# Kernel optimization log

Hardware: AMD Instinct MI355X
Metric: run time of the kernel (lower is better)

The kernel has to match this reference:

```python
import jax, jax.numpy as jnp
import numpy as np

D = 1024
H = 16
HD = D // H  # 64
S = 2048
B = 1


def setup_inputs() -> dict:
    key = jax.random.key(0)
    ks = jax.random.split(key, 6)
    return {
        "GLO": jax.random.normal(ks[0], (B, S, D), dtype=jnp.float32),
        "LOC": jax.random.normal(ks[1], (B, S, D), dtype=jnp.float32),
        "W_q": jax.random.normal(ks[2], (H, D, HD), dtype=jnp.float32),
        "W_k": jax.random.normal(ks[3], (H, D, HD), dtype=jnp.float32),
        "W_v": jax.random.normal(ks[4], (H, D, HD), dtype=jnp.float32),
        "W_o": jax.random.normal(ks[5], (H * HD, D), dtype=jnp.float32),
    }


def _cross_attn(q_src, kv_src, W_q, W_k, W_v, W_o):
    # q_src: [B,Sq,D], kv_src: [B,Sk,D]
    b, sq, _ = q_src.shape
    Q = jnp.einsum('bsd,hde->bhse', q_src, W_q)   # [B,H,Sq,hd]
    K = jnp.einsum('bsd,hde->bhse', kv_src, W_k)  # [B,H,Sk,hd]
    V = jnp.einsum('bsd,hde->bhse', kv_src, W_v)  # [B,H,Sk,hd]
    scores = jnp.einsum('bhqe,bhke->bhqk', Q, K) / jnp.sqrt(jnp.float32(HD))
    weights = jax.nn.softmax(scores, axis=-1)
    out = jnp.einsum('bhqk,bhke->bhqe', weights, V)  # [B,H,Sq,hd]
    # Faithful to torch .view (raw memory reinterpretation, no head transpose)
    out = out.reshape(b, sq, H * HD)
    return out @ W_o  # [B,Sq,D]


def reference(GLO, LOC, W_q, W_k, W_v, W_o):
    GLO_prime = _cross_attn(GLO, LOC, W_q, W_k, W_v, W_o)
    LOC_prime = _cross_attn(LOC, GLO, W_q, W_k, W_v, W_o)
    return (GLO_prime, LOC_prime)
```

## Files before the change

### kernel.cpp

```cpp
#include <hip/hip_runtime.h>
#include <math.h>

#define S_LEN 2048
#define D_DIM 1024
#define NH 16
#define HD 64

typedef __attribute__((ext_vector_type(8))) short bf16x8;
typedef __attribute__((ext_vector_type(4))) float f32x4;

#define MFMA(a, b, c) __builtin_amdgcn_mfma_f32_16x16x32_bf16((a), (b), (c), 0, 0, 0)

__device__ __forceinline__ unsigned short f2bf(float x) {
    unsigned int u = __float_as_uint(x);
    u = (u + 0x7FFFu + ((u >> 16) & 1u)) >> 16;
    return (unsigned short)u;
}
__device__ __forceinline__ float bf2f(unsigned short b) {
    return __uint_as_float(((unsigned int)b) << 16);
}
__device__ __forceinline__ void gl_lds16(const void* g, void* l) {
    __builtin_amdgcn_global_load_lds((const __attribute__((address_space(1))) unsigned int*)g,
                                     (__attribute__((address_space(3))) unsigned int*)l, 16, 0, 0);
}

#if defined(__has_builtin)
#if __has_builtin(__builtin_amdgcn_cvt_pk_bf16_f32)
#define HAVE_CVT_PK_BF16 1
#endif
#endif
__device__ __forceinline__ unsigned pack_bf16(float a, float b) {
#ifdef HAVE_CVT_PK_BF16
    auto r = __builtin_amdgcn_cvt_pk_bf16_f32(a, b);
    unsigned u;
    __builtin_memcpy(&u, &r, 4);
    return u;
#else
    unsigned ua = __float_as_uint(a) + 0x8000u;
    unsigned ub = __float_as_uint(b) + 0x8000u;
    return __builtin_amdgcn_perm(ub, ua, 0x07060302u);
#endif
}


__global__ __launch_bounds__(256) void prep(const float* __restrict__ GLO,
                                            const float* __restrict__ LOC,
                                            const float* __restrict__ Wq,
                                            const float* __restrict__ Wk,
                                            const float* __restrict__ Wv,
                                            const float* __restrict__ Wo,
                                            unsigned short* __restrict__ Xh,
                                            unsigned short* __restrict__ Xl,
                                            unsigned short* __restrict__ Wqh,
                                            unsigned short* __restrict__ Wql,
                                            unsigned short* __restrict__ Wkh,
                                            unsigned short* __restrict__ Wkl,
                                            unsigned short* __restrict__ Wvt,
                                            unsigned short* __restrict__ Wot) {
    int idx = blockIdx.x * 256 + threadIdx.x;
    if (idx < (1 << 19)) {
        int gg = idx & 7;
        int row = (idx >> 3) & 127;
        int kblk = (idx >> 10) & 15;
        int r = (idx >> 14) * 128 + row;
        int kg = gg ^ (row & 7);
        const float* src = (r & 2048) ? LOC : GLO;
        const float* sp = src + (size_t)(r & 2047) * 1024 + kblk * 64 + kg * 8;
        float4 x0 = *(const float4*)sp;
        float4 x1 = *(const float4*)(sp + 4);
        size_t t = (size_t)idx * 8;
        ushort4 h0, l0, h1, l1;
        h0.x = f2bf(x0.x); l0.x = f2bf(x0.x - bf2f(h0.x));
        h0.y = f2bf(x0.y); l0.y = f2bf(x0.y - bf2f(h0.y));
        h0.z = f2bf(x0.z); l0.z = f2bf(x0.z - bf2f(h0.z));
        h0.w = f2bf(x0.w); l0.w = f2bf(x0.w - bf2f(h0.w));
        h1.x = f2bf(x1.x); l1.x = f2bf(x1.x - bf2f(h1.x));
        h1.y = f2bf(x1.y); l1.y = f2bf(x1.y - bf2f(h1.y));
        h1.z = f2bf(x1.z); l1.z = f2bf(x1.z - bf2f(h1.z));
        h1.w = f2bf(x1.w); l1.w = f2bf(x1.w - bf2f(h1.w));
        *(ushort4*)(Xh + t) = h0;
        *(ushort4*)(Xh + t + 4) = h1;
        *(ushort4*)(Xl + t) = l0;
        *(ushort4*)(Xl + t + 4) = l1;
    } else {
        int idx2 = idx - (1 << 19);
        int sec = idx2 >> 17;
        int j = idx2 & 0x1FFFF;
        size_t t = (size_t)j * 8;
        if (sec < 3) {
            int gg = j & 7;
            int e = (j >> 3) & 63;
            int kblk = (j >> 9) & 15;
            int head = j >> 13;
            int kg = gg ^ (e & 7);
            int d0 = kblk * 64 + kg * 8;
            const float* W = (sec == 0) ? Wq : (sec == 1) ? Wk : Wv;
            const float* wp = W + (size_t)head * 65536 + (size_t)d0 * 64 + e;
            float wv8[8];
#pragma unroll
            for (int i = 0; i < 8; ++i) wv8[i] = wp[i * 64];
            if (sec == 0) {
                ushort4 h0, l0, h1, l1;
#pragma unroll
                for (int i = 0; i < 8; ++i) {
                    float v = wv8[i] * 0.18033688011112042f;
                    unsigned short hi = f2bf(v);
                    unsigned short lo = f2bf(v - bf2f(hi));
                    if (i < 4) {
                        ((unsigned short*)&h0)[i] = hi;
                        ((unsigned short*)&l0)[i] = lo;
                    } else {
                        ((unsigned short*)&h1)[i - 4] = hi;
                        ((unsigned short*)&l1)[i - 4] = lo;
                    }
                }
                *(ushort4*)(Wqh + t) = h0;
                *(ushort4*)(Wqh + t + 4) = h1;
                *(ushort4*)(Wql + t) = l0;
                *(ushort4*)(Wql + t + 4) = l1;
            } else if (sec == 1) {
                ushort4 h0, l0, h1, l1;
#pragma unroll
                for (int i = 0; i < 8; ++i) {
                    float v = wv8[i];
                    unsigned short hi = f2bf(v);
                    unsigned short lo = f2bf(v - bf2f(hi));
                    if (i < 4) {
                        ((unsigned short*)&h0)[i] = hi;
                        ((unsigned short*)&l0)[i] = lo;
                    } else {
                        ((unsigned short*)&h1)[i - 4] = hi;
                        ((unsigned short*)&l1)[i - 4] = lo;
                    }
                }
                *(ushort4*)(Wkh + t) = h0;
                *(ushort4*)(Wkh + t + 4) = h1;
                *(ushort4*)(Wkl + t) = l0;
                *(ushort4*)(Wkl + t + 4) = l1;
            } else {
                ushort4 v0, v1;
#pragma unroll
                for (int i = 0; i < 8; ++i) {
                    unsigned short b = f2bf(wv8[i]);
                    if (i < 4)
                        ((unsigned short*)&v0)[i] = b;
                    else
                        ((unsigned short*)&v1)[i - 4] = b;
                }
                *(ushort4*)(Wvt + t) = v0;
                *(ushort4*)(Wvt + t + 4) = v1;
            }
        } else {
            int gg = j & 7;
            int col = (j >> 3) & 63;
            int kblk = (j >> 9) & 15;
            int nblk = j >> 13;
            int kg = gg ^ (col & 7);
            int k0 = kblk * 64 + kg * 8;
            int n = nblk * 64 + col;
            ushort4 v0, v1;
#pragma unroll
            for (int i = 0; i < 8; ++i) {
                unsigned short b = f2bf(Wo[(size_t)(k0 + i) * 1024 + n]);
                if (i < 4)
                    ((unsigned short*)&v0)[i] = b;
                else
                    ((unsigned short*)&v1)[i - 4] = b;
            }
            *(ushort4*)(Wot + t) = v0;
            *(ushort4*)(Wot + t + 4) = v1;
        }
    }
}

__global__ __launch_bounds__(256) void qkv_proj(const unsigned short* __restrict__ Xh,
                                                const unsigned short* __restrict__ Xl,
                                                const unsigned short* __restrict__ Wqh,
                                                const unsigned short* __restrict__ Wql,
                                                const unsigned short* __restrict__ Wkh,
                                                const unsigned short* __restrict__ Wkl,
                                                const unsigned short* __restrict__ Wvt,
                                                unsigned short* __restrict__ Qh,
                                                unsigned short* __restrict__ Ql,
                                                unsigned short* __restrict__ Kh,
                                                unsigned short* __restrict__ Kl,
                                                unsigned short* __restrict__ Vt) {
    __shared__ unsigned short lds[36864];
    const int bid = blockIdx.x;
    const int mblk = bid & 31;
    const int head = bid >> 5;
    const int tid = threadIdx.x;
    const int lane = tid & 63;
    const int w = tid >> 6;
    const int l15 = lane & 15, quad = lane >> 4;

    f32x4 aq[2][4] = {}, ak[2][4] = {}, av[2][4] = {};
    const size_t abase0 = (size_t)mblk * 131072;
    const size_t bbase0 = (size_t)head * 65536;

    for (int kb = 0; kb < 16; ++kb) {
        __syncthreads();
        {
            const size_t ab = abase0 + (size_t)kb * 8192;
            const size_t bb = bbase0 + (size_t)kb * 4096;
#pragma unroll
            for (int j = 0; j < 4; ++j) {
                int seg = j * 256 + tid;
                gl_lds16(Xh + ab + seg * 8, &lds[seg * 8]);
                gl_lds16(Xl + ab + seg * 8, &lds[8192 + seg * 8]);
            }
#pragma unroll
            for (int j = 0; j < 2; ++j) {
                int seg = j * 256 + tid;
                gl_lds16(Wqh + bb + seg * 8, &lds[16384 + seg * 8]);
                gl_lds16(Wql + bb + seg * 8, &lds[20480 + seg * 8]);
                gl_lds16(Wkh + bb + seg * 8, &lds[24576 + seg * 8]);
                gl_lds16(Wkl + bb + seg * 8, &lds[28672 + seg * 8]);
                gl_lds16(Wvt + bb + seg * 8, &lds[32768 + seg * 8]);
            }
        }
        __syncthreads();

#pragma unroll
        for (int ksub = 0; ksub < 2; ++ksub) {
            bf16x8 ah[2], al8[2];
#pragma unroll
            for (int mt = 0; mt < 2; ++mt) {
                int row = w * 32 + mt * 16 + l15;
                int g = (ksub * 4 + quad) ^ (row & 7);
                ah[mt] = *(const bf16x8*)&lds[row * 64 + g * 8];
                al8[mt] = *(const bf16x8*)&lds[8192 + row * 64 + g * 8];
            }
#pragma unroll
            for (int nt = 0; nt < 4; ++nt) {
                int col = nt * 16 + l15;
                int o = col * 64 + ((ksub * 4 + quad) ^ (col & 7)) * 8;
                bf16x8 bqh = *(const bf16x8*)&lds[16384 + o];
                bf16x8 bql = *(const bf16x8*)&lds[20480 + o];
                bf16x8 bkh = *(const bf16x8*)&lds[24576 + o];
                bf16x8 bkl = *(const bf16x8*)&lds[28672 + o];
                bf16x8 bv = *(const bf16x8*)&lds[32768 + o];
#pragma unroll
                for (int mt = 0; mt < 2; ++mt) {
                    f32x4 a = aq[mt][nt];
                    a = MFMA(ah[mt], bqh, a);
                    a = MFMA(ah[mt], bql, a);
                    a = MFMA(al8[mt], bqh, a);
                    aq[mt][nt] = a;
                    f32x4 b = ak[mt][nt];
                    b = MFMA(ah[mt], bkh, b);
                    b = MFMA(ah[mt], bkl, b);
                    b = MFMA(al8[mt], bkh, b);
                    ak[mt][nt] = b;
                    av[mt][nt] = MFMA(ah[mt], bv, av[mt][nt]);
                }
            }
        }
    }

#pragma unroll
    for (int mt = 0; mt < 2; ++mt) {
        const int rbase = mblk * 128 + w * 32 + mt * 16 + quad * 4;
#pragma unroll
        for (int nt = 0; nt < 4; ++nt) {
            const int col = head * 64 + nt * 16 + l15;
#pragma unroll
            for (int r = 0; r < 4; ++r) {
                size_t a = (size_t)(rbase + r) * D_DIM + col;
                float vq = aq[mt][nt][r];
                unsigned short hq = f2bf(vq);
                Qh[a] = hq;
                Ql[a] = f2bf(vq - bf2f(hq));
                float vk = ak[mt][nt][r];
                unsigned short hk = f2bf(vk);
                Kh[a] = hk;
                Kl[a] = f2bf(vk - bf2f(hk));
            }
            ushort4 vp;
            vp.x = f2bf(av[mt][nt][0]);
            vp.y = f2bf(av[mt][nt][1]);
            vp.z = f2bf(av[mt][nt][2]);
            vp.w = f2bf(av[mt][nt][3]);
            *(ushort4*)(Vt + (size_t)col * (2 * S_LEN) + rbase) = vp;
        }
    }
}

__global__ __launch_bounds__(256, 4) void attn_kernel(const unsigned short* __restrict__ Qh_,
                                                      const unsigned short* __restrict__ Ql_,
                                                      const unsigned short* __restrict__ Kh_,
                                                      const unsigned short* __restrict__ Kl_,
                                                      const unsigned short* __restrict__ Vt_,
                                                      unsigned short* __restrict__ Opart,
                                                      float* __restrict__ Lse) {
    __shared__ unsigned short lds[16384];
    const int bid = blockIdx.x;
    const int qblk = bid & 15;
    const int head = (bid >> 4) & 15;
    const int dir = (bid >> 8) & 1;
    const int khalf = bid >> 9;
    const int src_q = dir, src_kv = 1 - dir;

    const int tid = threadIdx.x;
    const int lane = tid & 63;
    const int w = tid >> 6;
    const int l15 = lane & 15, quad = lane >> 4;
    const int q0w = qblk * 128 + w * 32;

    const unsigned short* KhB0 =
        Kh_ + (size_t)(src_kv * S_LEN + khalf * 1024) * D_DIM + head * 64;
    const unsigned short* KlB0 =
        Kl_ + (size_t)(src_kv * S_LEN + khalf * 1024) * D_DIM + head * 64;
    const unsigned short* Vtp =
        Vt_ + (size_t)(head * 64) * (2 * S_LEN) + src_kv * S_LEN + khalf * 1024;

    auto stage = [&](int k0) {
#pragma unroll
        for (int j = 0; j < 2; ++j) {
            int i = j * 256 + tid;
            int row = i >> 3;
            int col = ((i & 7) ^ (row & 7)) * 8;
            gl_lds16(KhB0 + (size_t)(k0 + row) * D_DIM + col, &lds[i * 8]);
            gl_lds16(KlB0 + (size_t)(k0 + row) * D_DIM + col, &lds[4096 + i * 8]);
            gl_lds16(Vtp + (size_t)row * (2 * S_LEN) + k0 + col, &lds[8192 + i * 8]);
        }
    };

    bf16x8 qh[2][2], ql[2][2];
#pragma unroll
    for (int mt = 0; mt < 2; ++mt) {
        const size_t qrow =
            (size_t)(src_q * S_LEN + q0w + mt * 16 + l15) * D_DIM + head * 64 + quad * 8;
#pragma unroll
        for (int c = 0; c < 2; ++c) {
            qh[mt][c] = *(const bf16x8*)(Qh_ + qrow + c * 32);
            ql[mt][c] = *(const bf16x8*)(Ql_ + qrow + c * 32);
        }
    }

    f32x4 o[2][4] = {};
    float mi[2] = {-1e30f, -1e30f};
    float lip[2] = {0.f, 0.f};
    unsigned short* Pw = lds + 12288 + w * 1024;

    auto chunk = [&]() {
        f32x4 sa[2][4];
        __builtin_amdgcn_s_setprio(1);
#pragma unroll
        for (int kt = 0; kt < 4; ++kt) {
            const int row = kt * 16 + l15;
            const int s0 = (quad ^ (row & 7)) * 8;
            const int s1 = ((4 + quad) ^ (row & 7)) * 8;
            bf16x8 kh0 = *(const bf16x8*)&lds[row * 64 + s0];
            bf16x8 kh1 = *(const bf16x8*)&lds[row * 64 + s1];
            bf16x8 kl0 = *(const bf16x8*)&lds[4096 + row * 64 + s0];
            bf16x8 kl1 = *(const bf16x8*)&lds[4096 + row * 64 + s1];
#pragma unroll
            for (int mt = 0; mt < 2; ++mt) {
                f32x4 a = {};
                a = MFMA(kh0, qh[mt][0], a);
                a = MFMA(kh1, qh[mt][1], a);
                a = MFMA(kl0, qh[mt][0], a);
                a = MFMA(kl1, qh[mt][1], a);
                a = MFMA(kh0, ql[mt][0], a);
                a = MFMA(kh1, ql[mt][1], a);
                sa[mt][kt] = a;
            }
        }
        __builtin_amdgcn_s_setprio(0);

#pragma unroll
        for (int mt = 0; mt < 2; ++mt) {
            f32x4 t4 = __builtin_elementwise_max(__builtin_elementwise_max(sa[mt][0], sa[mt][1]),
                                                 __builtin_elementwise_max(sa[mt][2], sa[mt][3]));
            float tm = fmaxf(fmaxf(t4[0], t4[1]), fmaxf(t4[2], t4[3]));
            tm = fmaxf(tm, __shfl_xor(tm, 16, 64));
            tm = fmaxf(tm, __shfl_xor(tm, 32, 64));
            if (__ballot(tm > mi[mt])) {
                float mn = fmaxf(mi[mt], tm);
                float al = exp2f(mi[mt] - mn);
                mi[mt] = mn;
                lip[mt] *= al;
                const f32x4 alv = {al, al, al, al};
#pragma unroll
                for (int et = 0; et < 4; ++et) o[mt][et] *= alv;
            }
            const float mn = mi[mt];
            const f32x4 mnv = {mn, mn, mn, mn};
            f32x4 rs4 = {};
#pragma unroll
            for (int kt = 0; kt < 4; ++kt) {
                f32x4 p = sa[mt][kt] - mnv;
#pragma unroll
                for (int r = 0; r < 4; ++r) p[r] = exp2f(p[r]);
                rs4 += p;
                uint2 pk;
                pk.x = pack_bf16(p[0], p[1]);
                pk.y = pack_bf16(p[2], p[3]);
                int g = (kt * 2 + (quad >> 1)) ^ (l15 & 7);
                *(uint2*)&Pw[l15 * 64 + g * 8 + (quad & 1) * 4] = pk;
            }
            lip[mt] += (rs4[0] + rs4[1]) + (rs4[2] + rs4[3]);

            __builtin_amdgcn_s_setprio(1);
#pragma unroll
            for (int c = 0; c < 2; ++c) {
                bf16x8 pf = *(const bf16x8*)&Pw[l15 * 64 + (((c * 4 + quad) ^ (l15 & 7)) * 8)];
#pragma unroll
                for (int et = 0; et < 4; ++et) {
                    const int row = et * 16 + l15;
                    const int sl = ((c * 4 + quad) ^ (row & 7)) * 8;
                    bf16x8 vf = *(const bf16x8*)&lds[8192 + row * 64 + sl];
                    o[mt][et] = MFMA(vf, pf, o[mt][et]);
                }
            }
            __builtin_amdgcn_s_setprio(0);
        }
    };

#pragma unroll 1
    for (int c = 0; c < 16; ++c) {
        __syncthreads();
        stage(c * 64);
        __syncthreads();
        chunk();
    }

    const size_t pbase = (size_t)(khalf * 32 + dir * 16 + head) * 2048;
#pragma unroll
    for (int mt = 0; mt < 2; ++mt) {
        float lq = lip[mt];
        lq += __shfl_xor(lq, 16, 64);
        lq += __shfl_xor(lq, 32, 64);
        const float rl = __builtin_amdgcn_rcpf(lq);
        const int q = qblk * 128 + w * 32 + mt * 16 + l15;
        const size_t ob = (pbase + q) * 64;
#pragma unroll
        for (int et = 0; et < 4; ++et) {
            ushort4 pk;
            pk.x = f2bf(o[mt][et][0] * rl);
            pk.y = f2bf(o[mt][et][1] * rl);
            pk.z = f2bf(o[mt][et][2] * rl);
            pk.w = f2bf(o[mt][et][3] * rl);
            *(ushort4*)(Opart + ob + et * 16 + quad * 4) = pk;
        }
        if (quad == 0) Lse[pbase + q] = mi[mt] + __log2f(lq);
    }
}

__global__ __launch_bounds__(256) void combine(const unsigned short* __restrict__ Opart,
                                               const float* __restrict__ Lse,
                                               unsigned short* __restrict__ Oatt) {
    const int t = blockIdx.x * 256 + threadIdx.x;
    const int qi = t >> 3;
    const int e0 = (t & 7) * 8;
    const int dh = qi >> 11;
    const int q = qi & 2047;

    const size_t row1 = (size_t)dh * 2048 + q;
    const size_t b1 = row1 * 64 + e0;
    const size_t b2 = b1 + (size_t)4194304;
    ushort4 p1a = *(const ushort4*)(Opart + b1);
    ushort4 p1b = *(const ushort4*)(Opart + b1 + 4);
    ushort4 p2a = *(const ushort4*)(Opart + b2);
    ushort4 p2b = *(const ushort4*)(Opart + b2 + 4);
    const float l1 = Lse[row1];
    const float l2 = Lse[row1 + 65536];

    const float M = fmaxf(l1, l2);
    float w1 = exp2f(l1 - M);
    float w2 = exp2f(l2 - M);
    const float rw = __builtin_amdgcn_rcpf(w1 + w2);
    w1 *= rw;
    w2 *= rw;

    ushort4 oa, ob;
    oa.x = f2bf(bf2f(p1a.x) * w1 + bf2f(p2a.x) * w2);
    oa.y = f2bf(bf2f(p1a.y) * w1 + bf2f(p2a.y) * w2);
    oa.z = f2bf(bf2f(p1a.z) * w1 + bf2f(p2a.z) * w2);
    oa.w = f2bf(bf2f(p1a.w) * w1 + bf2f(p2a.w) * w2);
    ob.x = f2bf(bf2f(p1b.x) * w1 + bf2f(p2b.x) * w2);
    ob.y = f2bf(bf2f(p1b.y) * w1 + bf2f(p2b.y) * w2);
    ob.z = f2bf(bf2f(p1b.z) * w1 + bf2f(p2b.z) * w2);
    ob.w = f2bf(bf2f(p1b.w) * w1 + bf2f(p2b.w) * w2);

    const int rowit = q >> 4;
    const int g = ((e0 >> 3) ^ (rowit & 7)) & 7;
    const size_t oaddr =
        (size_t)dh * 131072 + (size_t)(q & 15) * 8192 + (size_t)rowit * 64 + g * 8;
    *(ushort4*)(Oatt + oaddr) = oa;
    *(ushort4*)(Oatt + oaddr + 4) = ob;
}

__global__ __launch_bounds__(256) void oproj(const unsigned short* __restrict__ Oatt,
                                             const unsigned short* __restrict__ Wot,
                                             float* __restrict__ out) {
    __shared__ unsigned short lds[24576];
    const int bid = blockIdx.x;
    const int nblk = bid & 15;
    const int mblk = bid >> 4;
    const int tid = threadIdx.x;
    const int lane = tid & 63, w = tid >> 6, l15 = lane & 15, quad = lane >> 4;

    f32x4 acc[2][4] = {};
    const size_t abase = (size_t)mblk * 131072;
    const size_t bbase = (size_t)nblk * 65536;

    auto ostage = [&](int kb, int boff) {
#pragma unroll
        for (int j = 0; j < 4; ++j) {
            int seg = j * 256 + tid;
            gl_lds16(Oatt + abase + (size_t)kb * 8192 + seg * 8, &lds[boff + seg * 8]);
        }
#pragma unroll
        for (int j = 0; j < 2; ++j) {
            int seg = j * 256 + tid;
            gl_lds16(Wot + bbase + (size_t)kb * 4096 + seg * 8, &lds[boff + 8192 + seg * 8]);
        }
    };

    auto compute = [&](int boff) {
#pragma unroll
        for (int ksub = 0; ksub < 2; ++ksub) {
            bf16x8 a[2];
#pragma unroll
            for (int mt = 0; mt < 2; ++mt) {
                int row = w * 32 + mt * 16 + l15;
                a[mt] =
                    *(const bf16x8*)&lds[boff + row * 64 + (((ksub * 4 + quad) ^ (row & 7)) * 8)];
            }
#pragma unroll
            for (int nt = 0; nt < 4; ++nt) {
                int col = nt * 16 + l15;
                bf16x8 b = *(const bf16x8*)&lds[boff + 8192 + col * 64 +
                                                (((ksub * 4 + quad) ^ (col & 7)) * 8)];
#pragma unroll
                for (int mt = 0; mt < 2; ++mt) acc[mt][nt] = MFMA(a[mt], b, acc[mt][nt]);
            }
        }
    };

    ostage(0, 0);
#pragma unroll 1
    for (int kb = 0; kb < 16; kb += 2) {
        __syncthreads();
        if (kb + 1 < 16) ostage(kb + 1, 12288);
        compute(0);
        __syncthreads();
        if (kb + 2 < 16) ostage(kb + 2, 0);
        compute(12288);
    }

#pragma unroll
    for (int mt = 0; mt < 2; ++mt) {
        const int rbase = mblk * 128 + w * 32 + mt * 16 + quad * 4;
#pragma unroll
        for (int nt = 0; nt < 4; ++nt)
#pragma unroll
            for (int r = 0; r < 4; ++r)
                out[(size_t)(rbase + r) * D_DIM + nblk * 64 + nt * 16 + l15] = acc[mt][nt][r];
    }
}

extern "C" void kernel_launch(void* const* d_in, const int* in_sizes, int n_in, void* d_out,
                              int out_size, void* d_ws, size_t ws_size, hipStream_t stream) {
    const float* GLO = (const float*)d_in[0];
    const float* LOC = (const float*)d_in[1];
    const float* Wq = (const float*)d_in[2];
    const float* Wk = (const float*)d_in[3];
    const float* Wv = (const float*)d_in[4];
    const float* Wo = (const float*)d_in[5];
    float* out = (float*)d_out;

    unsigned short* ws = (unsigned short*)d_ws;
    unsigned short* Xh = ws + 0;
    unsigned short* Xl = ws + 4194304;
    unsigned short* Wqh = ws + 8388608;
    unsigned short* Wql = ws + 9437184;
    unsigned short* Wkh = ws + 10485760;
    unsigned short* Wkl = ws + 11534336;
    unsigned short* Wvt = ws + 12582912;
    unsigned short* Wot = ws + 13631488;
    unsigned short* Qh = ws + 14680064;
    unsigned short* Ql = ws + 18874368;
    unsigned short* Kh = ws + 23068672;
    unsigned short* Kl = ws + 27262976;
    unsigned short* Vt = ws + 31457280;
    unsigned short* Oatt = ws + 35651584;
    unsigned short* Opart = ws + 0;
    float* LseP = (float*)(ws + 8388608);

    prep<<<4096, 256, 0, stream>>>(GLO, LOC, Wq, Wk, Wv, Wo, Xh, Xl, Wqh, Wql, Wkh, Wkl, Wvt, Wot);
    qkv_proj<<<512, 256, 0, stream>>>(Xh, Xl, Wqh, Wql, Wkh, Wkl, Wvt, Qh, Ql, Kh, Kl, Vt);
    attn_kernel<<<1024, 256, 0, stream>>>(Qh, Ql, Kh, Kl, Vt, Opart, LseP);
    combine<<<2048, 256, 0, stream>>>(Opart, LseP, Oatt);
    oproj<<<512, 256, 0, stream>>>(Oatt, Wot, out);
}
```

Baseline: 269.7 us.

## Double-buffer K/V tiles in attention with 32-key chunks and one barrier per step

Restructures the attention main loop to prefetch the next K chunk (32 keys) and V chunk (64 keys) into alternate LDS buffers, so there is one barrier per iteration instead of two and global loads overlap compute. The chunk size for scores drops to 32 keys, which halves P scratch and puts V fragments in registers. The block index mapping also changes so consecutive blocks share the same q block and differ in head, direction and key half, which changes L2 reuse. LDS per block grows, and the online-softmax rescale check now runs twice as often.

```diff
diff --git a/kernel.cpp b/kernel.cpp
--- a/kernel.cpp
+++ b/kernel.cpp
@@ -293,12 +293,13 @@
                                                       const unsigned short* __restrict__ Vt_,
                                                       unsigned short* __restrict__ Opart,
                                                       float* __restrict__ Lse) {
-    __shared__ unsigned short lds[16384];
+    __shared__ unsigned short lds[18432];
     const int bid = blockIdx.x;
-    const int qblk = bid & 15;
-    const int head = (bid >> 4) & 15;
-    const int dir = (bid >> 8) & 1;
-    const int khalf = bid >> 9;
+    const int rlow = bid & 63;
+    const int head = rlow & 15;
+    const int dir = (rlow >> 4) & 1;
+    const int khalf = rlow >> 5;
+    const int qblk = bid >> 6;
     const int src_q = dir, src_kv = 1 - dir;
 
     const int tid = threadIdx.x;
@@ -314,15 +315,19 @@
     const unsigned short* Vtp =
         Vt_ + (size_t)(head * 64) * (2 * S_LEN) + src_kv * S_LEN + khalf * 1024;
 
-    auto stage = [&](int k0) {
+    const int rowK = tid >> 3;
+    const int colK = ((tid & 7) ^ (rowK & 7)) * 8;
+    auto stageK = [&](int k0, int kboff) {
+        gl_lds16(KhB0 + (size_t)(k0 + rowK) * D_DIM + colK, &lds[kboff + tid * 8]);
+        gl_lds16(KlB0 + (size_t)(k0 + rowK) * D_DIM + colK, &lds[kboff + 2048 + tid * 8]);
+    };
+    auto stageV = [&](int v0, int vboff) {
 #pragma unroll
         for (int j = 0; j < 2; ++j) {
             int i = j * 256 + tid;
             int row = i >> 3;
             int col = ((i & 7) ^ (row & 7)) * 8;
-            gl_lds16(KhB0 + (size_t)(k0 + row) * D_DIM + col, &lds[i * 8]);
-            gl_lds16(KlB0 + (size_t)(k0 + row) * D_DIM + col, &lds[4096 + i * 8]);
-            gl_lds16(Vtp + (size_t)row * (2 * S_LEN) + k0 + col, &lds[8192 + i * 8]);
+            gl_lds16(Vtp + (size_t)row * (2 * S_LEN) + v0 + col, &lds[vboff + i * 8]);
         }
     };
 
@@ -341,20 +346,30 @@
     f32x4 o[2][4] = {};
     float mi[2] = {-1e30f, -1e30f};
     float lip[2] = {0.f, 0.f};
-    unsigned short* Pw = lds + 12288 + w * 1024;
-
-    auto chunk = [&]() {
-        f32x4 sa[2][4];
+    unsigned short* Pw = lds + 16384 + w * 512;
+
+    stageK(0, 0);
+    stageV(0, 8192);
+#pragma unroll 1
+    for (int kd = 0; kd < 32; ++kd) {
+        __syncthreads();
+        if (kd + 1 < 32) stageK((kd + 1) * 32, (kd & 1) ? 0 : 4096);
+        if (!(kd & 1) && (kd / 2 + 1 < 16)) stageV((kd / 2 + 1) * 64, (kd & 2) ? 8192 : 12288);
+        const int kb = (kd & 1) ? 4096 : 0;
+        const int vb = ((kd >> 1) & 1) ? 12288 : 8192;
+        const int p = kd & 1;
+
+        f32x4 sa[2][2];
         __builtin_amdgcn_s_setprio(1);
 #pragma unroll
-        for (int kt = 0; kt < 4; ++kt) {
+        for (int kt = 0; kt < 2; ++kt) {
             const int row = kt * 16 + l15;
             const int s0 = (quad ^ (row & 7)) * 8;
             const int s1 = ((4 + quad) ^ (row & 7)) * 8;
-            bf16x8 kh0 = *(const bf16x8*)&lds[row * 64 + s0];
-            bf16x8 kh1 = *(const bf16x8*)&lds[row * 64 + s1];
-            bf16x8 kl0 = *(const bf16x8*)&lds[4096 + row * 64 + s0];
-            bf16x8 kl1 = *(const bf16x8*)&lds[4096 + row * 64 + s1];
+            bf16x8 kh0 = *(const bf16x8*)&lds[kb + row * 64 + s0];
+            bf16x8 kh1 = *(const bf16x8*)&lds[kb + row * 64 + s1];
+            bf16x8 kl0 = *(const bf16x8*)&lds[kb + 2048 + row * 64 + s0];
+            bf16x8 kl1 = *(const bf16x8*)&lds[kb + 2048 + row * 64 + s1];
 #pragma unroll
             for (int mt = 0; mt < 2; ++mt) {
                 f32x4 a = {};
@@ -369,10 +384,16 @@
         }
         __builtin_amdgcn_s_setprio(0);
 
+        bf16x8 vf[4];
+#pragma unroll
+        for (int et = 0; et < 4; ++et) {
+            const int row = et * 16 + l15;
+            vf[et] = *(const bf16x8*)&lds[vb + row * 64 + (((p * 4 + quad) ^ (row & 7)) * 8)];
+        }
+
 #pragma unroll
         for (int mt = 0; mt < 2; ++mt) {
-            f32x4 t4 = __builtin_elementwise_max(__builtin_elementwise_max(sa[mt][0], sa[mt][1]),
-                                                 __builtin_elementwise_max(sa[mt][2], sa[mt][3]));
+            f32x4 t4 = __builtin_elementwise_max(sa[mt][0], sa[mt][1]);
             float tm = fmaxf(fmaxf(t4[0], t4[1]), fmaxf(t4[2], t4[3]));
             tm = fmaxf(tm, __shfl_xor(tm, 16, 64));
             tm = fmaxf(tm, __shfl_xor(tm, 32, 64));
@@ -389,41 +410,25 @@
             const f32x4 mnv = {mn, mn, mn, mn};
             f32x4 rs4 = {};
 #pragma unroll
-            for (int kt = 0; kt < 4; ++kt) {
-                f32x4 p = sa[mt][kt] - mnv;
-#pragma unroll
-                for (int r = 0; r < 4; ++r) p[r] = exp2f(p[r]);
-                rs4 += p;
+            for (int kt = 0; kt < 2; ++kt) {
+                f32x4 pv = sa[mt][kt] - mnv;
+#pragma unroll
+                for (int r = 0; r < 4; ++r) pv[r] = exp2f(pv[r]);
+                rs4 += pv;
                 uint2 pk;
-                pk.x = pack_bf16(p[0], p[1]);
-                pk.y = pack_bf16(p[2], p[3]);
-                int g = (kt * 2 + (quad >> 1)) ^ (l15 & 7);
-                *(uint2*)&Pw[l15 * 64 + g * 8 + (quad & 1) * 4] = pk;
+                pk.x = pack_bf16(pv[0], pv[1]);
+                pk.y = pack_bf16(pv[2], pv[3]);
+                int g = (kt * 2 + (quad >> 1)) ^ (l15 & 3);
+                *(uint2*)&Pw[l15 * 32 + g * 8 + (quad & 1) * 4] = pk;
             }
             lip[mt] += (rs4[0] + rs4[1]) + (rs4[2] + rs4[3]);
 
+            bf16x8 pf = *(const bf16x8*)&Pw[l15 * 32 + ((quad ^ (l15 & 3)) * 8)];
             __builtin_amdgcn_s_setprio(1);
 #pragma unroll
-            for (int c = 0; c < 2; ++c) {
-                bf16x8 pf = *(const bf16x8*)&Pw[l15 * 64 + (((c * 4 + quad) ^ (l15 & 7)) * 8)];
-#pragma unroll
-                for (int et = 0; et < 4; ++et) {
-                    const int row = et * 16 + l15;
-                    const int sl = ((c * 4 + quad) ^ (row & 7)) * 8;
-                    bf16x8 vf = *(const bf16x8*)&lds[8192 + row * 64 + sl];
-                    o[mt][et] = MFMA(vf, pf, o[mt][et]);
-                }
-            }
+            for (int et = 0; et < 4; ++et) o[mt][et] = MFMA(vf[et], pf, o[mt][et]);
             __builtin_amdgcn_s_setprio(0);
         }
-    };
-
-#pragma unroll 1
-    for (int c = 0; c < 16; ++c) {
-        __syncthreads();
-        stage(c * 64);
-        __syncthreads();
-        chunk();
     }
 
     const size_t pbase = (size_t)(khalf * 32 + dir * 16 + head) * 2048;
```

Result: faster. 263.2 us (-2.4%).

## Double-buffer attention K/V staging with 512-thread blocks and lazy softmax rescale

Applied to the files above, without the earlier changes.

The attention kernel moves to 512-thread blocks covering 256 queries, with a double-buffered LDS ring, so the next K/V chunk's global-to-LDS load overlaps the current chunk's compute. Each block's K/V chunk is now shared by twice as many query rows. Online-softmax rescaling is skipped unless the running max grows by more than 8 (log2 units), which cuts rescale work but lets exponentials reach up to 2^8 before rescaling. The block-index mapping is reordered in both the attention and o-projection kernels, presumably to improve cache locality, and the setprio hints are removed. The doubled LDS and larger blocks may lower occupancy.

```diff
diff --git a/kernel.cpp b/kernel.cpp
--- a/kernel.cpp
+++ b/kernel.cpp
@@ -286,26 +286,26 @@
     }
 }
 
-__global__ __launch_bounds__(256, 4) void attn_kernel(const unsigned short* __restrict__ Qh_,
+__global__ __launch_bounds__(512, 4) void attn_kernel(const unsigned short* __restrict__ Qh_,
                                                       const unsigned short* __restrict__ Ql_,
                                                       const unsigned short* __restrict__ Kh_,
                                                       const unsigned short* __restrict__ Kl_,
                                                       const unsigned short* __restrict__ Vt_,
                                                       unsigned short* __restrict__ Opart,
                                                       float* __restrict__ Lse) {
-    __shared__ unsigned short lds[16384];
+    __shared__ unsigned short lds[32768];
     const int bid = blockIdx.x;
-    const int qblk = bid & 15;
-    const int head = (bid >> 4) & 15;
-    const int dir = (bid >> 8) & 1;
-    const int khalf = bid >> 9;
+    const int head = bid & 15;
+    const int dir = (bid >> 4) & 1;
+    const int khalf = (bid >> 5) & 1;
+    const int qblk = bid >> 6;
     const int src_q = dir, src_kv = 1 - dir;
 
     const int tid = threadIdx.x;
     const int lane = tid & 63;
     const int w = tid >> 6;
     const int l15 = lane & 15, quad = lane >> 4;
-    const int q0w = qblk * 128 + w * 32;
+    const int q0w = qblk * 256 + w * 32;
 
     const unsigned short* KhB0 =
         Kh_ + (size_t)(src_kv * S_LEN + khalf * 1024) * D_DIM + head * 64;
@@ -314,16 +314,16 @@
     const unsigned short* Vtp =
         Vt_ + (size_t)(head * 64) * (2 * S_LEN) + src_kv * S_LEN + khalf * 1024;
 
-    auto stage = [&](int k0) {
-#pragma unroll
-        for (int j = 0; j < 2; ++j) {
-            int i = j * 256 + tid;
-            int row = i >> 3;
-            int col = ((i & 7) ^ (row & 7)) * 8;
-            gl_lds16(KhB0 + (size_t)(k0 + row) * D_DIM + col, &lds[i * 8]);
-            gl_lds16(KlB0 + (size_t)(k0 + row) * D_DIM + col, &lds[4096 + i * 8]);
-            gl_lds16(Vtp + (size_t)row * (2 * S_LEN) + k0 + col, &lds[8192 + i * 8]);
-        }
+    const int i0 = tid;
+    const int sr0 = i0 >> 3, sc0 = ((i0 & 7) ^ (sr0 & 7)) * 8;
+
+    auto stage = [&](int k0, int boff) {
+        const unsigned short* KhB = KhB0 + (size_t)k0 * D_DIM;
+        const unsigned short* KlB = KlB0 + (size_t)k0 * D_DIM;
+        const unsigned short* VB = Vtp + k0;
+        gl_lds16(KhB + (size_t)sr0 * D_DIM + sc0, &lds[boff + i0 * 8]);
+        gl_lds16(KlB + (size_t)sr0 * D_DIM + sc0, &lds[boff + 4096 + i0 * 8]);
+        gl_lds16(VB + (size_t)sr0 * (2 * S_LEN) + sc0, &lds[boff + 8192 + i0 * 8]);
     };
 
     bf16x8 qh[2][2], ql[2][2];
@@ -341,20 +341,19 @@
     f32x4 o[2][4] = {};
     float mi[2] = {-1e30f, -1e30f};
     float lip[2] = {0.f, 0.f};
-    unsigned short* Pw = lds + 12288 + w * 1024;
-
-    auto chunk = [&]() {
+    unsigned short* Pw = lds + 24576 + w * 1024;
+
+    auto chunk = [&](int kb) {
         f32x4 sa[2][4];
-        __builtin_amdgcn_s_setprio(1);
 #pragma unroll
         for (int kt = 0; kt < 4; ++kt) {
             const int row = kt * 16 + l15;
             const int s0 = (quad ^ (row & 7)) * 8;
             const int s1 = ((4 + quad) ^ (row & 7)) * 8;
-            bf16x8 kh0 = *(const bf16x8*)&lds[row * 64 + s0];
-            bf16x8 kh1 = *(const bf16x8*)&lds[row * 64 + s1];
-            bf16x8 kl0 = *(const bf16x8*)&lds[4096 + row * 64 + s0];
-            bf16x8 kl1 = *(const bf16x8*)&lds[4096 + row * 64 + s1];
+            bf16x8 kh0 = *(const bf16x8*)&lds[kb + row * 64 + s0];
+            bf16x8 kh1 = *(const bf16x8*)&lds[kb + row * 64 + s1];
+            bf16x8 kl0 = *(const bf16x8*)&lds[kb + 4096 + row * 64 + s0];
+            bf16x8 kl1 = *(const bf16x8*)&lds[kb + 4096 + row * 64 + s1];
 #pragma unroll
             for (int mt = 0; mt < 2; ++mt) {
                 f32x4 a = {};
@@ -367,7 +366,6 @@
                 sa[mt][kt] = a;
             }
         }
-        __builtin_amdgcn_s_setprio(0);
 
 #pragma unroll
         for (int mt = 0; mt < 2; ++mt) {
@@ -376,7 +374,7 @@
             float tm = fmaxf(fmaxf(t4[0], t4[1]), fmaxf(t4[2], t4[3]));
             tm = fmaxf(tm, __shfl_xor(tm, 16, 64));
             tm = fmaxf(tm, __shfl_xor(tm, 32, 64));
-            if (__ballot(tm > mi[mt])) {
+            if (__ballot(tm > mi[mt] + 8.f)) {
                 float mn = fmaxf(mi[mt], tm);
                 float al = exp2f(mi[mt] - mn);
                 mi[mt] = mn;
@@ -402,7 +400,6 @@
             }
             lip[mt] += (rs4[0] + rs4[1]) + (rs4[2] + rs4[3]);
 
-            __builtin_amdgcn_s_setprio(1);
 #pragma unroll
             for (int c = 0; c < 2; ++c) {
                 bf16x8 pf = *(const bf16x8*)&Pw[l15 * 64 + (((c * 4 + quad) ^ (l15 & 7)) * 8)];
@@ -410,20 +407,22 @@
                 for (int et = 0; et < 4; ++et) {
                     const int row = et * 16 + l15;
                     const int sl = ((c * 4 + quad) ^ (row & 7)) * 8;
-                    bf16x8 vf = *(const bf16x8*)&lds[8192 + row * 64 + sl];
+                    bf16x8 vf = *(const bf16x8*)&lds[kb + 8192 + row * 64 + sl];
                     o[mt][et] = MFMA(vf, pf, o[mt][et]);
                 }
             }
-            __builtin_amdgcn_s_setprio(0);
         }
     };
 
+    stage(0, 0);
 #pragma unroll 1
-    for (int c = 0; c < 16; ++c) {
+    for (int kd = 0; kd < 16; kd += 2) {
         __syncthreads();
-        stage(c * 64);
+        if (kd + 1 < 16) stage((kd + 1) * 64, 12288);
+        chunk(0);
         __syncthreads();
-        chunk();
+        if (kd + 2 < 16) stage((kd + 2) * 64, 0);
+        chunk(12288);
     }
 
     const size_t pbase = (size_t)(khalf * 32 + dir * 16 + head) * 2048;
@@ -433,7 +432,7 @@
         lq += __shfl_xor(lq, 16, 64);
         lq += __shfl_xor(lq, 32, 64);
         const float rl = __builtin_amdgcn_rcpf(lq);
-        const int q = qblk * 128 + w * 32 + mt * 16 + l15;
+        const int q = q0w + mt * 16 + l15;
         const size_t ob = (pbase + q) * 64;
 #pragma unroll
         for (int et = 0; et < 4; ++et) {
@@ -497,8 +496,8 @@
                                              float* __restrict__ out) {
     __shared__ unsigned short lds[24576];
     const int bid = blockIdx.x;
-    const int nblk = bid & 15;
-    const int mblk = bid >> 4;
+    const int mblk = bid & 31;
+    const int nblk = bid >> 5;
     const int tid = threadIdx.x;
     const int lane = tid & 63, w = tid >> 6, l15 = lane & 15, quad = lane >> 4;
 
@@ -592,7 +591,7 @@
 
     prep<<<4096, 256, 0, stream>>>(GLO, LOC, Wq, Wk, Wv, Wo, Xh, Xl, Wqh, Wql, Wkh, Wkl, Wvt, Wot);
     qkv_proj<<<512, 256, 0, stream>>>(Xh, Xl, Wqh, Wql, Wkh, Wkl, Wvt, Qh, Ql, Kh, Kl, Vt);
-    attn_kernel<<<1024, 256, 0, stream>>>(Qh, Ql, Kh, Kl, Vt, Opart, LseP);
+    attn_kernel<<<512, 512, 0, stream>>>(Qh, Ql, Kh, Kl, Vt, Opart, LseP);
     combine<<<2048, 256, 0, stream>>>(Opart, LseP, Oatt);
     oproj<<<512, 256, 0, stream>>>(Oatt, Wot, out);
 }
```

Result: slower. 300.7 us (+11.5%).
